# Performance work log

Hardware: AMD Instinct MI355X
Metric: run time of the kernel (lower is better)

## Reference

```python
import jax, jax.numpy as jnp
import numpy as np

B = 1
L_IMG, L_TMP, L_TXT = 1024, 1024, 256
D, H, HD, MLP = 1024, 16, 64, 4096
L = L_TXT + L_IMG + L_TMP
EPS = 1e-6
ATTN_SCALE = float(1.0 / np.sqrt(HD))


def setup_inputs() -> dict:
    key = jax.random.key(0)
    ks = jax.random.split(key, 12)
    s = 0.02  # keep activations stable
    return {
        'img': jax.random.normal(ks[0], (B, L_IMG, D), jnp.float32),
        'temporal': jax.random.normal(ks[1], (B, L_TMP, D), jnp.float32),
        'txt': jax.random.normal(ks[2], (B, L_TXT, D), jnp.float32),
        'vec': jax.random.normal(ks[3], (B, D), jnp.float32),
        'pe': jax.random.normal(ks[4], (B, 1, L, HD // 2, 2, 2), jnp.float32),
        'mod_w': jax.random.normal(ks[5], (3, D, 6 * D), jnp.float32) * s,
        'mod_b': jnp.zeros((3, 6 * D), jnp.float32),
        'qkv_w': jax.random.normal(ks[6], (3, D, 3 * D), jnp.float32) * s,
        'q_scale': jnp.ones((3, HD), jnp.float32),
        'k_scale': jnp.ones((3, HD), jnp.float32),
        'proj_w': jax.random.normal(ks[7], (3, D, D), jnp.float32) * s,
        'proj_b': jnp.zeros((3, D), jnp.float32),
        'mlp_w1': jax.random.normal(ks[8], (3, D, MLP), jnp.float32) * s,
        'mlp_b1': jnp.zeros((3, MLP), jnp.float32),
        'mlp_w2': jax.random.normal(ks[9], (3, MLP, D), jnp.float32) * s,
        'mlp_b2': jnp.zeros((3, D), jnp.float32),
    }


def _ln(x):
    # LayerNorm, elementwise_affine=False, eps=1e-6
    m = jnp.mean(x, axis=-1, keepdims=True)
    v = jnp.mean((x - m) ** 2, axis=-1, keepdims=True)
    return (x - m) * jax.lax.rsqrt(v + EPS)


def _rms(x, scale):
    # flux QKNorm RMSNorm with learnable per-head-dim scale
    return x * jax.lax.rsqrt(jnp.mean(x * x, axis=-1, keepdims=True) + EPS) * scale


def _rope(x, pe):
    # x: (B,H,L,HD), pe: (B,1,L,HD//2,2,2)
    xr = x.reshape(*x.shape[:-1], -1, 1, 2)
    out = pe[..., 0] * xr[..., 0] + pe[..., 1] * xr[..., 1]  # (B,H,L,HD//2,2)
    return out.reshape(x.shape)


def _forward(img, temporal, txt, vec, pe, mod_w, mod_b, qkv_w, q_scale, k_scale,
             proj_w, proj_b, mlp_w1, mlp_b1, mlp_w2, mlp_b2):
    sv = jax.nn.silu(vec)  # (B,D)

    def mods(i):
        m = (sv @ mod_w[i] + mod_b[i])[:, None, :]  # (B,1,6D)
        return jnp.split(m, 6, axis=-1)  # shift1, scale1, gate1, shift2, scale2, gate2

    def qkv_stream(x, i, shift1, scale1):
        xm = (1.0 + scale1) * _ln(x) + shift1
        qkv = (xm @ qkv_w[i]).reshape(x.shape[0], x.shape[1], 3, H, HD)
        q, k, v = jnp.moveaxis(qkv, 2, 0)  # each (B,Ls,H,HD)
        q = jnp.swapaxes(q, 1, 2)
        k = jnp.swapaxes(k, 1, 2)
        v = jnp.swapaxes(v, 1, 2)  # (B,H,Ls,HD)
        return _rms(q, q_scale[i]), _rms(k, k_scale[i]), v

    i_sh1, i_sc1, i_g1, i_sh2, i_sc2, i_g2 = mods(0)
    t_sh1, t_sc1, t_g1, t_sh2, t_sc2, t_g2 = mods(1)
    x_sh1, x_sc1, x_g1, x_sh2, x_sc2, x_g2 = mods(2)

    img_q, img_k, img_v = qkv_stream(img, 0, i_sh1, i_sc1)
    tmp_q, tmp_k, tmp_v = qkv_stream(temporal, 1, t_sh1, t_sc1)
    txt_q, txt_k, txt_v = qkv_stream(txt, 2, x_sh1, x_sc1)

    q = jnp.concatenate((txt_q, img_q, tmp_q), axis=2)
    k = jnp.concatenate((txt_k, img_k, tmp_k), axis=2)
    # NOTE: faithful to source bug: v concat uses temporal_q, not temporal_v
    v = jnp.concatenate((txt_v, img_v, tmp_q), axis=2)

    q = _rope(q, pe)
    k = _rope(k, pe)
    scores = jnp.einsum('bhqd,bhkd->bhqk', q, k) * ATTN_SCALE
    attn = jnp.einsum('bhqk,bhkd->bhqd', jax.nn.softmax(scores, axis=-1), v)
    attn = jnp.swapaxes(attn, 1, 2).reshape(attn.shape[0], L, H * HD)  # (B,L,D)

    txt_a = attn[:, :L_TXT]
    img_a = attn[:, L_TXT:L_TXT + L_IMG]
    tmp_a = attn[:, L_TXT + L_IMG:]

    def mlp(x, i):
        return jax.nn.gelu(x @ mlp_w1[i] + mlp_b1[i], approximate=True) @ mlp_w2[i] + mlp_b2[i]

    img = img + i_g1 * (img_a @ proj_w[0] + proj_b[0])
    img = img + i_g2 * mlp((1.0 + i_sc2) * _ln(img) + i_sh2, 0)
    temporal = temporal + t_g1 * (tmp_a @ proj_w[1] + proj_b[1])
    # NOTE: faithful to source bug: temporal_norm2 is applied to (updated) img
    temporal = temporal + t_g2 * mlp((1.0 + t_sc2) * _ln(img) + t_sh2, 1)
    txt = txt + x_g1 * (txt_a @ proj_w[2] + proj_b[2])
    txt = txt + x_g2 * mlp((1.0 + x_sc2) * _ln(txt) + x_sh2, 2)
    return img, temporal, txt


def reference(img, temporal, txt, vec, pe, mod_w, mod_b, qkv_w, q_scale, k_scale,
              proj_w, proj_b, mlp_w1, mlp_b1, mlp_w2, mlp_b2):
    return _forward(img, temporal, txt, vec, pe, mod_w, mod_b, qkv_w, q_scale,
                    k_scale, proj_w, proj_b, mlp_w1, mlp_b1, mlp_w2, mlp_b2)
```

## Files before the change

### kernel.cpp

```cpp
#include <hip/hip_runtime.h>
#include <hip/hip_bf16.h>

#define L_TXT 256
#define L_IMG 1024
#define L_TMP 1024
#define LTOT  2304
#define DMODEL 1024
#define NH 16
#define HDIM 64
#define DMLP 4096
#define EPSV 1e-6f

typedef unsigned short ushort;
typedef __attribute__((ext_vector_type(8))) short short8b;
typedef __attribute__((ext_vector_type(8))) unsigned short ushort8v;
typedef __attribute__((ext_vector_type(4))) float f32x4;
typedef __attribute__((ext_vector_type(4))) unsigned short ushort4v;

#define MOD_OFF    ((size_t)0)
#define XM_OFF     ((size_t)73728)
#define QKV_OFF    ((size_t)4792320)
#define QB_OFF     ((size_t)18948096)
#define KB_OFF     ((size_t)23666688)
#define VTB_OFF    ((size_t)28385280)
#define ATT_OFF    ((size_t)33103872)
#define S1_OFF     ((size_t)37822464)
#define QKVWT_OFF  ((size_t)49356800)
#define PROJWT_OFF ((size_t)68231168)
#define W1T_OFF    ((size_t)74522624)
#define W2T_OFF    ((size_t)99688448)
#define W2T_END    ((size_t)124854272)

static __device__ __forceinline__ ushort f2bf(float x) {
    __hip_bfloat16 b = __float2bfloat16(x);
    return *reinterpret_cast<ushort*>(&b);
}
static __device__ __forceinline__ float bf2f(ushort u) {
    return __uint_as_float(((unsigned)u) << 16);
}

typedef __attribute__((address_space(1))) const unsigned char gas_t;
typedef __attribute__((address_space(3))) unsigned char las_t;
static __device__ __forceinline__ void gload16(const void* g, void* l) {
    __builtin_amdgcn_global_load_lds((gas_t*)g, (las_t*)l, 16, 0, 0);
}

__global__ __launch_bounds__(256) void k_wt_all(const float* __restrict__ vec,
                                                const float* __restrict__ modw,
                                                const float* __restrict__ modb,
                                                float* __restrict__ mod,
                                                const float* __restrict__ qkvw,
                                                const float* __restrict__ projw,
                                                const float* __restrict__ w1,
                                                const float* __restrict__ w2,
                                                ushort* __restrict__ qkvwt,
                                                ushort* __restrict__ projwt,
                                                ushort* __restrict__ w1t,
                                                ushort* __restrict__ w2t) {
    __shared__ float tb[32][33];
    __shared__ float svs[DMODEL];
    __shared__ float pl[8][128];
    int bid = blockIdx.x;
    int tid = threadIdx.x;
    if (bid < 144) {
        float4 vv = *reinterpret_cast<const float4*>(vec + tid*4);
        float4 sv4;
        sv4.x = vv.x / (1.0f + __expf(-vv.x));
        sv4.y = vv.y / (1.0f + __expf(-vv.y));
        sv4.z = vv.z / (1.0f + __expf(-vv.z));
        sv4.w = vv.w / (1.0f + __expf(-vv.w));
        *reinterpret_cast<float4*>(&svs[tid*4]) = sv4;
        __syncthreads();
        int g0 = bid * 128;
        int i  = g0 / 6144;
        int j0 = g0 - i * 6144;
        int jl = tid & 31, ko = tid >> 5;
        const float* wp = modw + (size_t)i * 1024 * 6144 + j0 + jl*4;
        float4 acc = {0.f,0.f,0.f,0.f};
        for (int kk = 0; kk < 128; kk++) {
            int k = kk*8 + ko;
            float4 wv = *reinterpret_cast<const float4*>(wp + (size_t)k * 6144);
            float s = svs[k];
            acc.x += s*wv.x; acc.y += s*wv.y; acc.z += s*wv.z; acc.w += s*wv.w;
        }
        pl[ko][jl*4+0] = acc.x; pl[ko][jl*4+1] = acc.y;
        pl[ko][jl*4+2] = acc.z; pl[ko][jl*4+3] = acc.w;
        __syncthreads();
        if (tid < 128) {
            float s = 0.f;
#pragma unroll
            for (int k = 0; k < 8; k++) s += pl[k][tid];
            mod[g0 + tid] = s + modb[g0 + tid];
        }
        return;
    }
    bid -= 144;
    const float* W; ushort* WT; int K, N;
    if (bid < 9216) {
        int s = bid / 3072, r = bid % 3072;
        K = 1024; N = 3072;
        W = qkvw + (size_t)s * K * N; WT = qkvwt + (size_t)s * N * K;
        bid = r;
    } else if (bid < 12288) {
        int b = bid - 9216; int s = b / 1024, r = b % 1024;
        K = 1024; N = 1024;
        W = projw + (size_t)s * K * N; WT = projwt + (size_t)s * N * K;
        bid = r;
    } else if (bid < 24576) {
        int b = bid - 12288; int s = b / 4096, r = b % 4096;
        K = 1024; N = 4096;
        W = w1 + (size_t)s * K * N; WT = w1t + (size_t)s * N * K;
        bid = r;
    } else {
        int b = bid - 24576; int s = b / 4096, r = b % 4096;
        K = 4096; N = 1024;
        W = w2 + (size_t)s * K * N; WT = w2t + (size_t)s * N * K;
        bid = r;
    }
    int nt = bid % (N >> 5), kt = bid / (N >> 5);
    int r = tid >> 5, c = tid & 31;
#pragma unroll
    for (int i = 0; i < 4; i++)
        tb[r + i*8][c] = W[(size_t)(kt*32 + r + i*8) * N + nt*32 + c];
    __syncthreads();
#pragma unroll
    for (int i = 0; i < 4; i++)
        WT[(size_t)(nt*32 + r + i*8) * K + kt*32 + c] = f2bf(tb[c][r + i*8]);
}

__global__ __launch_bounds__(256) void k_wt_slice(const float* __restrict__ W,
                                                  ushort* __restrict__ WT,
                                                  int K, int N) {
    int nt = blockIdx.x, kt = blockIdx.y;
    __shared__ float tb[32][33];
    int r = threadIdx.x >> 5, c = threadIdx.x & 31;
#pragma unroll
    for (int i = 0; i < 4; i++)
        tb[r + i*8][c] = W[(size_t)(kt*32 + r + i*8) * N + nt*32 + c];
    __syncthreads();
#pragma unroll
    for (int i = 0; i < 4; i++)
        WT[(size_t)(nt*32 + r + i*8) * K + kt*32 + c] = f2bf(tb[c][r + i*8]);
}

__global__ __launch_bounds__(256) void k_ln_mod1(const float* __restrict__ img,
                                                 const float* __restrict__ tmp,
                                                 const float* __restrict__ txt,
                                                 const float* __restrict__ mod,
                                                 ushort* __restrict__ xm) {
    int l = blockIdx.x;
    const float* src; int strm;
    if (l < L_TXT)              { src = txt + (size_t)l * DMODEL;            strm = 2; }
    else if (l < L_TXT + L_IMG) { src = img + (size_t)(l - L_TXT) * DMODEL;  strm = 0; }
    else                        { src = tmp + (size_t)(l - L_TXT - L_IMG) * DMODEL; strm = 1; }

    int d = threadIdx.x * 4;
    float4 x = *reinterpret_cast<const float4*>(src + d);
    float s  = x.x + x.y + x.z + x.w;
    float s2 = x.x*x.x + x.y*x.y + x.z*x.z + x.w*x.w;
#pragma unroll
    for (int o = 32; o > 0; o >>= 1) { s += __shfl_xor(s, o); s2 += __shfl_xor(s2, o); }
    __shared__ float red[8];
    int wave = threadIdx.x >> 6, lane = threadIdx.x & 63;
    if (lane == 0) { red[wave*2] = s; red[wave*2+1] = s2; }
    __syncthreads();
    if (threadIdx.x == 0) {
        float a = 0.f, b = 0.f;
        for (int w = 0; w < 4; w++) { a += red[w*2]; b += red[w*2+1]; }
        red[0] = a; red[1] = b;
    }
    __syncthreads();
    float mean = red[0] * (1.0f/DMODEL);
    float var  = red[1] * (1.0f/DMODEL) - mean*mean;
    float inv  = rsqrtf(var + EPSV);

    const float* sh = mod + strm*6144;
    const float* sc = sh + 1024;
    float4 shv = *reinterpret_cast<const float4*>(sh + d);
    float4 scv = *reinterpret_cast<const float4*>(sc + d);
    ushort4v o;
    o.x = f2bf((1.f+scv.x)*((x.x-mean)*inv) + shv.x);
    o.y = f2bf((1.f+scv.y)*((x.y-mean)*inv) + shv.y);
    o.z = f2bf((1.f+scv.z)*((x.z-mean)*inv) + shv.z);
    o.w = f2bf((1.f+scv.w)*((x.w-mean)*inv) + shv.w);
    *reinterpret_cast<ushort4v*>(xm + (size_t)l*DMODEL + d) = o;
}

__global__ __launch_bounds__(256) void k_ln_mod2(const float* __restrict__ src,
                                                 const float* __restrict__ sh,
                                                 const float* __restrict__ sc,
                                                 ushort* __restrict__ out) {
    int r = blockIdx.x;
    const float* srow = src + (size_t)r * DMODEL;
    int d = threadIdx.x * 4;
    float4 x = *reinterpret_cast<const float4*>(srow + d);
    float s  = x.x + x.y + x.z + x.w;
    float s2 = x.x*x.x + x.y*x.y + x.z*x.z + x.w*x.w;
#pragma unroll
    for (int o = 32; o > 0; o >>= 1) { s += __shfl_xor(s, o); s2 += __shfl_xor(s2, o); }
    __shared__ float red[8];
    int wave = threadIdx.x >> 6, lane = threadIdx.x & 63;
    if (lane == 0) { red[wave*2] = s; red[wave*2+1] = s2; }
    __syncthreads();
    if (threadIdx.x == 0) {
        float a = 0.f, b = 0.f;
        for (int w = 0; w < 4; w++) { a += red[w*2]; b += red[w*2+1]; }
        red[0] = a; red[1] = b;
    }
    __syncthreads();
    float mean = red[0] * (1.0f/DMODEL);
    float var  = red[1] * (1.0f/DMODEL) - mean*mean;
    float inv  = rsqrtf(var + EPSV);
    float4 shv = *reinterpret_cast<const float4*>(sh + d);
    float4 scv = *reinterpret_cast<const float4*>(sc + d);
    ushort4v o;
    o.x = f2bf((1.f+scv.x)*((x.x-mean)*inv) + shv.x);
    o.y = f2bf((1.f+scv.y)*((x.y-mean)*inv) + shv.y);
    o.z = f2bf((1.f+scv.z)*((x.z-mean)*inv) + shv.z);
    o.w = f2bf((1.f+scv.w)*((x.w-mean)*inv) + shv.w);
    *reinterpret_cast<ushort4v*>(out + (size_t)r*DMODEL + d) = o;
}

__device__ __forceinline__ float gelu_fast(float x) {
    return x / (1.0f + __expf(-1.5957691216057308f * (x + 0.044715f * x * x * x)));
}

template<int MODE, int BM, typename OutT>
__global__ __launch_bounds__(256) void k_gemm_ms(const ushort* __restrict__ A_t,
                                                 const ushort* __restrict__ A_i,
                                                 const ushort* __restrict__ A_m,
                                                 const ushort* __restrict__ BT,
                                                 const float* __restrict__ bias,
                                                 const float* __restrict__ res_t,
                                                 const float* __restrict__ res_i,
                                                 const float* __restrict__ res_m,
                                                 const float* __restrict__ mod, int gidx,
                                                 OutT* __restrict__ out_t,
                                                 OutT* __restrict__ out_i,
                                                 OutT* __restrict__ out_m,
                                                 int N, int K, int ry0) {
    constexpr int MI = BM / 32;
    const int brow = (ry0 + blockIdx.y) * BM;
    int s, lrow;
    if (brow < 256)       { s = 2; lrow = brow; }
    else if (brow < 1280) { s = 0; lrow = brow - 256; }
    else                  { s = 1; lrow = brow - 1280; }

    const ushort* A = (s==2 ? A_t : s==0 ? A_i : A_m) + (size_t)lrow * K;
    const ushort* BTs = BT + (size_t)s * N * K;
    const float* bi = bias ? bias + (size_t)s * N : nullptr;
    const float* resl = (MODE==2) ? ((s==2 ? res_t : s==0 ? res_i : res_m) + (size_t)lrow * N) : nullptr;
    const float* gate = (MODE==2) ? (mod + s*6144 + gidx*1024) : nullptr;
    OutT* Cl = (s==2 ? out_t : s==0 ? out_i : out_m) + (size_t)lrow * N;

    __shared__ ushort Asl[BM*64];
    __shared__ ushort Bsl[128*64];
    const int tid = threadIdx.x;
    const int lane = tid & 63, w = tid >> 6;
    const int wr = w >> 1, wc = w & 1;
    const int bn = blockIdx.x * 128;
    const int r15 = lane & 15, g4 = lane >> 4;

    f32x4 acc[MI][4];
#pragma unroll
    for (int i = 0; i < MI; i++)
#pragma unroll
        for (int j = 0; j < 4; j++) acc[i][j] = (f32x4){0.f,0.f,0.f,0.f};

    for (int k0 = 0; k0 < K; k0 += 64) {
#pragma unroll
        for (int i = 0; i < BM/32; i++) {
            int chunk = i*4 + w;
            int seg = chunk*64 + lane;
            int row = seg >> 3;
            int gs  = (seg & 7) ^ (row & 7);
            gload16(A + (size_t)row * K + k0 + gs*8, Asl + (size_t)chunk * 512);
        }
#pragma unroll
        for (int i = 0; i < 4; i++) {
            int chunk = i*4 + w;
            int seg = chunk*64 + lane;
            int row = seg >> 3;
            int gs  = (seg & 7) ^ (row & 7);
            gload16(BTs + (size_t)(bn + row) * K + k0 + gs*8, Bsl + (size_t)chunk * 512);
        }
        __syncthreads();
#pragma unroll
        for (int kk = 0; kk < 2; kk++) {
            short8b a[MI], b[4];
#pragma unroll
            for (int mi = 0; mi < MI; mi++) {
                int row = wr*(MI*16) + mi*16 + r15;
                int c   = kk*4 + g4;
                a[mi] = *reinterpret_cast<const short8b*>(&Asl[row*64 + ((c ^ (row & 7)))*8]);
            }
#pragma unroll
            for (int ni = 0; ni < 4; ni++) {
                int row = wc*64 + ni*16 + r15;
                int c   = kk*4 + g4;
                b[ni] = *reinterpret_cast<const short8b*>(&Bsl[row*64 + ((c ^ (row & 7)))*8]);
            }
#pragma unroll
            for (int mi = 0; mi < MI; mi++)
#pragma unroll
                for (int ni = 0; ni < 4; ni++)
                    acc[mi][ni] = __builtin_amdgcn_mfma_f32_16x16x32_bf16(a[mi], b[ni], acc[mi][ni], 0, 0, 0);
        }
        __syncthreads();
    }

#pragma unroll
    for (int mi = 0; mi < MI; mi++) {
#pragma unroll
        for (int ni = 0; ni < 4; ni++) {
            int col = bn + wc*64 + ni*16 + r15;
            float bv = bi ? bi[col] : 0.f;
#pragma unroll
            for (int r = 0; r < 4; r++) {
                int rr = wr*(MI*16) + mi*16 + g4*4 + r;
                float v = acc[mi][ni][r] + bv;
                if (MODE == 1) v = gelu_fast(v);
                if (MODE == 2) v = resl[(size_t)rr * N + col] + gate[col] * v;
                if (sizeof(OutT) == 2) Cl[(size_t)rr * N + col] = (OutT)f2bf(v);
                else                   Cl[(size_t)rr * N + col] = (OutT)v;
            }
        }
    }
}

__global__ __launch_bounds__(256) void k_qkvfin(const ushort* __restrict__ qkv,
                                                const float* __restrict__ pe,
                                                const float* __restrict__ qs,
                                                const float* __restrict__ ks,
                                                ushort* __restrict__ Q,
                                                ushort* __restrict__ K,
                                                ushort* __restrict__ Vt) {
    int wid  = (blockIdx.x * 256 + threadIdx.x) >> 6;
    int lane = threadIdx.x & 63;
    int l = wid >> 4;
    int h = wid & 15;
    int strm;
    if (l < L_TXT) strm = 2; else if (l < L_TXT + L_IMG) strm = 0; else strm = 1;

    const ushort* row = qkv + (size_t)l * 3 * DMODEL;
    float q = bf2f(row[h*HDIM + lane]);
    float k = bf2f(row[DMODEL + h*HDIM + lane]);
    float v = bf2f(row[2*DMODEL + h*HDIM + lane]);

    float sq = q*q, sk = k*k;
#pragma unroll
    for (int o = 32; o > 0; o >>= 1) { sq += __shfl_xor(sq, o); sk += __shfl_xor(sk, o); }
    float rq = q * rsqrtf(sq * (1.0f/HDIM) + EPSV) * qs[strm*HDIM + lane];
    float rk = k * rsqrtf(sk * (1.0f/HDIM) + EPSV) * ks[strm*HDIM + lane];

    float vout = (strm == 1) ? rq : v;

    float rq_p = __shfl_xor(rq, 1);
    float rk_p = __shfl_xor(rk, 1);
    float qe = (lane & 1) ? rq_p : rq;
    float qo = (lane & 1) ? rq : rq_p;
    float ke = (lane & 1) ? rk_p : rk;
    float ko = (lane & 1) ? rk : rk_p;
    const float* pel = pe + (size_t)l*128 + (lane >> 1)*4 + (lane & 1)*2;
    float qr = pel[0]*qe + pel[1]*qo;
    float kr = pel[0]*ke + pel[1]*ko;

    size_t idx = ((size_t)h * LTOT + l) * HDIM + lane;
    Q[idx] = f2bf(qr);
    K[idx] = f2bf(kr);
    Vt[idx] = f2bf(vout);
}

__global__ __launch_bounds__(256) void k_vt(const ushort* __restrict__ Vt,
                                            ushort* __restrict__ VT) {
    int h  = blockIdx.x >> 5;
    int lt = blockIdx.x & 31;
    if (lt >= 36) return;
    h = blockIdx.x / 36; lt = blockIdx.x % 36;
    int l0 = lt * 64;
    __shared__ ushort tbuf[64][72];
    int tid = threadIdx.x;
    {
        int l = tid >> 2, dc = (tid & 3) * 16;
        const ushort* src = Vt + ((size_t)NH*0 + (size_t)h * LTOT + l0 + l) * 64 + dc;
        ushort8v a = *reinterpret_cast<const ushort8v*>(src);
        ushort8v b = *reinterpret_cast<const ushort8v*>(src + 8);
#pragma unroll
        for (int i = 0; i < 8; i++) { tbuf[l][dc+i] = a[i]; tbuf[l][dc+8+i] = b[i]; }
    }
    __syncthreads();
    {
        int d = tid >> 2, lc = (tid & 3) * 16;
        ushort8v a, b;
#pragma unroll
        for (int i = 0; i < 8; i++) { a[i] = tbuf[lc+i][d]; b[i] = tbuf[lc+8+i][d]; }
        ushort* dst = VT + ((size_t)h * 64 + d) * LTOT + l0 + lc;
        *reinterpret_cast<ushort8v*>(dst) = a;
        *reinterpret_cast<ushort8v*>(dst + 8) = b;
    }
}

__global__ __launch_bounds__(256) void k_attn_mfma(const ushort* __restrict__ Qb,
                                                   const ushort* __restrict__ Kb,
                                                   const ushort* __restrict__ VTb,
                                                   ushort* __restrict__ att) {
    const int tid = threadIdx.x;
    const int w = tid >> 6, lane = tid & 63;
    const int h  = blockIdx.x / 36;
    const int qt = blockIdx.x % 36;
    const int qbase = qt*64 + w*16;
    const int g = lane >> 4;
    const int q = lane & 15;

    __shared__ ushort Ksl[64*64];
    __shared__ ushort Vsl[64*64];
    __shared__ ushort plds[4][1024];
    ushort* P = plds[w];

    const ushort* Kg = Kb  + (size_t)h * LTOT * 64;
    const ushort* Vg = VTb + (size_t)h * 64 * LTOT;

    const ushort* qp = Qb + ((size_t)h * LTOT + qbase + q) * 64 + g*8;
    const short8b qf0 = *reinterpret_cast<const short8b*>(qp);
    const short8b qf1 = *reinterpret_cast<const short8b*>(qp + 32);

    f32x4 out[4];
#pragma unroll
    for (int d = 0; d < 4; d++) out[d] = (f32x4){0.f,0.f,0.f,0.f};
    float m = -1e30f, lsum = 0.f;

    for (int kv0 = 0; kv0 < LTOT; kv0 += 64) {
#pragma unroll
        for (int i = 0; i < 2; i++) {
            int seg = i*256 + tid;
            int row = seg >> 3;
            int gs  = (seg & 7) ^ (row & 7);
            gload16(Kg + (size_t)(kv0 + row)*64 + gs*8, Ksl + (size_t)(i*256 + w*64)*8);
            gload16(Vg + (size_t)row*LTOT + kv0 + gs*8, Vsl + (size_t)(i*256 + w*64)*8);
        }
        __syncthreads();

        f32x4 s[4];
#pragma unroll
        for (int ks = 0; ks < 4; ks++) {
            int r = ks*16 + q;
            short8b kf0 = *reinterpret_cast<const short8b*>(&Ksl[r*64 + ((g     ^ (r & 7)))*8]);
            short8b kf1 = *reinterpret_cast<const short8b*>(&Ksl[r*64 + (((4+g) ^ (r & 7)))*8]);
            f32x4 acc = (f32x4){0.f,0.f,0.f,0.f};
            acc = __builtin_amdgcn_mfma_f32_16x16x32_bf16(kf0, qf0, acc, 0, 0, 0);
            acc = __builtin_amdgcn_mfma_f32_16x16x32_bf16(kf1, qf1, acc, 0, 0, 0);
            s[ks] = acc;
        }
        float tmax = -1e30f;
#pragma unroll
        for (int ks = 0; ks < 4; ks++)
#pragma unroll
            for (int r = 0; r < 4; r++) tmax = fmaxf(tmax, s[ks][r]);
        tmax = fmaxf(tmax, __shfl_xor(tmax, 16));
        tmax = fmaxf(tmax, __shfl_xor(tmax, 32));
        float newm = fmaxf(m, tmax * 0.125f);
        float c = __expf(m - newm);
        float p[16];
        float tsum = 0.f;
#pragma unroll
        for (int ks = 0; ks < 4; ks++)
#pragma unroll
            for (int r = 0; r < 4; r++) {
                float pv = __expf(s[ks][r] * 0.125f - newm);
                p[ks*4+r] = pv;
                tsum += pv;
            }
        tsum += __shfl_xor(tsum, 16);
        tsum += __shfl_xor(tsum, 32);
        lsum = lsum * c + tsum;
        m = newm;
#pragma unroll
        for (int d = 0; d < 4; d++) out[d] *= c;

#pragma unroll
        for (int ks = 0; ks < 4; ks++) {
            ushort4v pk;
            pk.x = f2bf(p[ks*4+0]); pk.y = f2bf(p[ks*4+1]);
            pk.z = f2bf(p[ks*4+2]); pk.w = f2bf(p[ks*4+3]);
            int widx = (q*64 + ks*16 + g*4) ^ ((q & 7) << 3);
            *reinterpret_cast<ushort4v*>(&P[widx]) = pk;
        }
#pragma unroll
        for (int c2 = 0; c2 < 2; c2++) {
            int ridx = (q*64 + c2*32 + g*8) ^ ((q & 7) << 3);
            short8b pf = *reinterpret_cast<const short8b*>(&P[ridx]);
#pragma unroll
            for (int ds = 0; ds < 4; ds++) {
                int d = ds*16 + q;
                short8b vf = *reinterpret_cast<const short8b*>(&Vsl[d*64 + (((c2*4+g) ^ (d & 7)))*8]);
                out[ds] = __builtin_amdgcn_mfma_f32_16x16x32_bf16(vf, pf, out[ds], 0, 0, 0);
            }
        }
        __syncthreads();
    }

    float inv = 1.0f / lsum;
    ushort* orow = att + (size_t)(qbase + q) * DMODEL + h * HDIM;
#pragma unroll
    for (int ds = 0; ds < 4; ds++) {
        ushort4v o4;
        o4.x = f2bf(out[ds][0]*inv); o4.y = f2bf(out[ds][1]*inv);
        o4.z = f2bf(out[ds][2]*inv); o4.w = f2bf(out[ds][3]*inv);
        *reinterpret_cast<ushort4v*>(orow + ds*16 + g*4) = o4;
    }
}

extern "C" void kernel_launch(void* const* d_in, const int* in_sizes, int n_in,
                              void* d_out, int out_size, void* d_ws, size_t ws_size,
                              hipStream_t stream) {
    const float* img  = (const float*)d_in[0];
    const float* tmp  = (const float*)d_in[1];
    const float* txt  = (const float*)d_in[2];
    const float* vec  = (const float*)d_in[3];
    const float* pe   = (const float*)d_in[4];
    const float* modw = (const float*)d_in[5];
    const float* modb = (const float*)d_in[6];
    const float* qkvw = (const float*)d_in[7];
    const float* qsc  = (const float*)d_in[8];
    const float* ksc  = (const float*)d_in[9];
    const float* projw= (const float*)d_in[10];
    const float* projb= (const float*)d_in[11];
    const float* w1   = (const float*)d_in[12];
    const float* b1   = (const float*)d_in[13];
    const float* w2   = (const float*)d_in[14];
    const float* b2   = (const float*)d_in[15];

    char* wsb = (char*)d_ws;
    float*  mod    = (float*) (wsb + MOD_OFF);
    ushort* xm     = (ushort*)(wsb + XM_OFF);
    ushort* qkv    = (ushort*)(wsb + QKV_OFF);
    ushort* t1     = (ushort*)(wsb + QKV_OFF);
    ushort* Qb     = (ushort*)(wsb + QB_OFF);
    ushort* Kb     = (ushort*)(wsb + KB_OFF);
    ushort* VTb    = (ushort*)(wsb + VTB_OFF);
    ushort* vtmp   = (ushort*)(wsb + ATT_OFF);
    ushort* att    = (ushort*)(wsb + ATT_OFF);
    float*  s1     = (float*) (wsb + S1_OFF);
    ushort* qkvwt  = (ushort*)(wsb + QKVWT_OFF);
    ushort* projwt = (ushort*)(wsb + PROJWT_OFF);
    ushort* w1t    = (ushort*)(wsb + W1T_OFF);

    const bool bigws = ws_size >= W2T_END;
    ushort* w2t = bigws ? (ushort*)(wsb + W2T_OFF) : w1t;

    float* out_img = (float*)d_out;
    float* out_tmp = out_img + (size_t)L_IMG * DMODEL;
    float* out_txt = out_tmp + (size_t)L_TMP * DMODEL;

    int wt_blocks = bigws ? (144 + 24576 + 12288) : (144 + 24576);
    k_wt_all<<<wt_blocks, 256, 0, stream>>>(vec, modw, modb, mod,
                                            qkvw, projw, w1, w2,
                                            qkvwt, projwt, w1t, w2t);
    k_ln_mod1<<<LTOT, 256, 0, stream>>>(img, tmp, txt, mod, xm);

    k_gemm_ms<0, 128, ushort><<<dim3(24, 18), 256, 0, stream>>>(
        xm, xm + (size_t)256*DMODEL, xm + (size_t)1280*DMODEL,
        qkvwt, nullptr, nullptr, nullptr, nullptr, nullptr, 0,
        qkv, qkv + (size_t)256*3072, qkv + (size_t)1280*3072, 3072, DMODEL, 0);

    k_qkvfin<<<9216, 256, 0, stream>>>(qkv, pe, qsc, ksc, Qb, Kb, vtmp);
    k_vt<<<NH*36, 256, 0, stream>>>(vtmp, VTb);
    k_attn_mfma<<<NH*36, 256, 0, stream>>>(Qb, Kb, VTb, att);

    k_gemm_ms<2, 64, float><<<dim3(8, 36), 256, 0, stream>>>(
        att, att + (size_t)256*DMODEL, att + (size_t)1280*DMODEL,
        projwt, projb, txt, img, tmp, mod, 2,
        s1, s1 + (size_t)256*DMODEL, s1 + (size_t)1280*DMODEL, DMODEL, DMODEL, 0);

    k_ln_mod2<<<L_TXT, 256, 0, stream>>>(s1,                        mod + 2*6144 + 3*1024, mod + 2*6144 + 4*1024, xm);
    k_ln_mod2<<<L_IMG, 256, 0, stream>>>(s1 + (size_t)256*DMODEL,   mod + 0*6144 + 3*1024, mod + 0*6144 + 4*1024, xm + (size_t)256*DMODEL);
    k_gemm_ms<1, 128, ushort><<<dim3(32, 10), 256, 0, stream>>>(
        xm, xm + (size_t)256*DMODEL, xm + (size_t)1280*DMODEL,
        w1t, b1, nullptr, nullptr, nullptr, nullptr, 0,
        t1, t1 + (size_t)256*DMLP, t1, DMLP, DMODEL, 0);
    if (!bigws) {
        k_wt_slice<<<dim3(32, 128), 256, 0, stream>>>(w2,                          w1t,                          DMLP, DMODEL);
        k_wt_slice<<<dim3(32, 128), 256, 0, stream>>>(w2 + (size_t)2*DMLP*DMODEL,  w1t + (size_t)2*DMLP*DMODEL,  DMLP, DMODEL);
    }
    k_gemm_ms<2, 64, float><<<dim3(8, 20), 256, 0, stream>>>(
        t1, t1 + (size_t)256*DMLP, t1,
        w2t, b2, s1, s1 + (size_t)256*DMODEL, s1 + (size_t)1280*DMODEL, mod, 5,
        out_txt, out_img, out_tmp, DMODEL, DMLP, 0);

    k_ln_mod2<<<L_TMP, 256, 0, stream>>>(out_img, mod + 1*6144 + 3*1024, mod + 1*6144 + 4*1024, xm + (size_t)1280*DMODEL);
    k_gemm_ms<1, 128, ushort><<<dim3(32, 8), 256, 0, stream>>>(
        xm, xm + (size_t)256*DMODEL, xm + (size_t)1280*DMODEL,
        w1t, b1, nullptr, nullptr, nullptr, nullptr, 0,
        t1, t1, t1, DMLP, DMODEL, 10);
    if (!bigws) {
        k_wt_slice<<<dim3(32, 128), 256, 0, stream>>>(w2 + (size_t)DMLP*DMODEL, w1t + (size_t)DMLP*DMODEL, DMLP, DMODEL);
    }
    k_gemm_ms<2, 64, float><<<dim3(8, 16), 256, 0, stream>>>(
        t1, t1, t1,
        w2t, b2, s1, s1, s1 + (size_t)1280*DMODEL, mod, 5,
        out_txt, out_img, out_tmp, DMODEL, DMLP, 20);
}
```

Measured before the change: 356.7 us.

## Widen weight transpose tiles, fuse V transpose, merge LN launches, double-buffer attention

The weight conversion kernels now use 64x64 tiles with float4 loads and 16-byte bf16 stores instead of 32x32 scalar tiles. The V transpose is folded into the QKV finalize kernel through an LDS buffer, which removes the separate k_vt launch and the intermediate round trip. The two LN-modulation launches are merged into one. The attention kernel double-buffers its K/V LDS tiles, prefetching the next tile while computing the current one, and adds s_setprio hints around the MFMA sections. Together these target transpose bandwidth, launch count and load latency in attention, at the cost of more LDS per block and fewer threads in qkvfin.

Measured after the change: 354.8 us. About the same (-0.5%).

```diff
diff --git a/kernel.cpp b/kernel.cpp
--- a/kernel.cpp
+++ b/kernel.cpp
@@ -45,24 +45,24 @@
     __builtin_amdgcn_global_load_lds((gas_t*)g, (las_t*)l, 16, 0, 0);
 }
 
-__global__ __launch_bounds__(256) void k_wt_all(const float* __restrict__ vec,
-                                                const float* __restrict__ modw,
-                                                const float* __restrict__ modb,
-                                                float* __restrict__ mod,
-                                                const float* __restrict__ qkvw,
-                                                const float* __restrict__ projw,
-                                                const float* __restrict__ w1,
-                                                const float* __restrict__ w2,
-                                                ushort* __restrict__ qkvwt,
-                                                ushort* __restrict__ projwt,
-                                                ushort* __restrict__ w1t,
-                                                ushort* __restrict__ w2t) {
-    __shared__ float tb[32][33];
-    __shared__ float svs[DMODEL];
-    __shared__ float pl[8][128];
+__global__ __launch_bounds__(256) void k_conv(const float* __restrict__ vec,
+                                              const float* __restrict__ modw,
+                                              const float* __restrict__ modb,
+                                              float* __restrict__ mod,
+                                              const float* __restrict__ qkvw,
+                                              const float* __restrict__ projw,
+                                              const float* __restrict__ w1,
+                                              const float* __restrict__ w2,
+                                              ushort* __restrict__ qkvwt,
+                                              ushort* __restrict__ projwt,
+                                              ushort* __restrict__ w1t,
+                                              ushort* __restrict__ w2t) {
+    __shared__ float tb[64][65];
     int bid = blockIdx.x;
     int tid = threadIdx.x;
     if (bid < 144) {
+        __shared__ float svs[DMODEL];
+        __shared__ float pl[8][128];
         float4 vv = *reinterpret_cast<const float4*>(vec + tid*4);
         float4 sv4;
         sv4.x = vv.x / (1.0f + __expf(-vv.x));
@@ -94,53 +94,74 @@
         }
         return;
     }
-    bid -= 144;
-    const float* W; ushort* WT; int K, N;
-    if (bid < 9216) {
-        int s = bid / 3072, r = bid % 3072;
-        K = 1024; N = 3072;
+    int b = bid - 144;
+    const float* W; ushort* WT; int K, N, nt, kt;
+    if (b < 2304) {
+        int s = b / 768, r = b % 768;
+        K = 1024; N = 3072; nt = r % 48; kt = r / 48;
         W = qkvw + (size_t)s * K * N; WT = qkvwt + (size_t)s * N * K;
-        bid = r;
-    } else if (bid < 12288) {
-        int b = bid - 9216; int s = b / 1024, r = b % 1024;
-        K = 1024; N = 1024;
+    } else if (b < 3072) {
+        b -= 2304; int s = b / 256, r = b % 256;
+        K = 1024; N = 1024; nt = r % 16; kt = r / 16;
         W = projw + (size_t)s * K * N; WT = projwt + (size_t)s * N * K;
-        bid = r;
-    } else if (bid < 24576) {
-        int b = bid - 12288; int s = b / 4096, r = b % 4096;
-        K = 1024; N = 4096;
+    } else if (b < 6144) {
+        b -= 3072; int s = b / 1024, r = b % 1024;
+        K = 1024; N = 4096; nt = r % 64; kt = r / 64;
         W = w1 + (size_t)s * K * N; WT = w1t + (size_t)s * N * K;
-        bid = r;
     } else {
-        int b = bid - 24576; int s = b / 4096, r = b % 4096;
-        K = 4096; N = 1024;
+        b -= 6144; int s = b / 1024, r = b % 1024;
+        K = 4096; N = 1024; nt = r % 16; kt = r / 16;
         W = w2 + (size_t)s * K * N; WT = w2t + (size_t)s * N * K;
-        bid = r;
-    }
-    int nt = bid % (N >> 5), kt = bid / (N >> 5);
-    int r = tid >> 5, c = tid & 31;
-#pragma unroll
-    for (int i = 0; i < 4; i++)
-        tb[r + i*8][c] = W[(size_t)(kt*32 + r + i*8) * N + nt*32 + c];
-    __syncthreads();
-#pragma unroll
-    for (int i = 0; i < 4; i++)
-        WT[(size_t)(nt*32 + r + i*8) * K + kt*32 + c] = f2bf(tb[c][r + i*8]);
-}
-
-__global__ __launch_bounds__(256) void k_wt_slice(const float* __restrict__ W,
-                                                  ushort* __restrict__ WT,
-                                                  int K, int N) {
-    int nt = blockIdx.x, kt = blockIdx.y;
-    __shared__ float tb[32][33];
-    int r = threadIdx.x >> 5, c = threadIdx.x & 31;
-#pragma unroll
-    for (int i = 0; i < 4; i++)
-        tb[r + i*8][c] = W[(size_t)(kt*32 + r + i*8) * N + nt*32 + c];
-    __syncthreads();
-#pragma unroll
-    for (int i = 0; i < 4; i++)
-        WT[(size_t)(nt*32 + r + i*8) * K + kt*32 + c] = f2bf(tb[c][r + i*8]);
+    }
+    {
+        int r = tid >> 4, c4 = (tid & 15) * 4;
+#pragma unroll
+        for (int i = 0; i < 4; i++) {
+            float4 v = *reinterpret_cast<const float4*>(W + (size_t)(kt*64 + r + i*16) * N + nt*64 + c4);
+            tb[r + i*16][c4+0] = v.x; tb[r + i*16][c4+1] = v.y;
+            tb[r + i*16][c4+2] = v.z; tb[r + i*16][c4+3] = v.w;
+        }
+    }
+    __syncthreads();
+    {
+        int n = tid >> 2, ks = (tid & 3) * 16;
+        ushort8v u0, u1;
+#pragma unroll
+        for (int i = 0; i < 8; i++) u0[i] = f2bf(tb[ks+i][n]);
+#pragma unroll
+        for (int i = 0; i < 8; i++) u1[i] = f2bf(tb[ks+8+i][n]);
+        ushort* dst = WT + (size_t)(nt*64 + n) * K + kt*64 + ks;
+        *reinterpret_cast<ushort8v*>(dst)     = u0;
+        *reinterpret_cast<ushort8v*>(dst + 8) = u1;
+    }
+}
+
+__global__ __launch_bounds__(256) void k_conv_slice(const float* __restrict__ W,
+                                                    ushort* __restrict__ WT,
+                                                    int K, int N) {
+    __shared__ float tb[64][65];
+    int nt = blockIdx.x, kt = blockIdx.y, tid = threadIdx.x;
+    {
+        int r = tid >> 4, c4 = (tid & 15) * 4;
+#pragma unroll
+        for (int i = 0; i < 4; i++) {
+            float4 v = *reinterpret_cast<const float4*>(W + (size_t)(kt*64 + r + i*16) * N + nt*64 + c4);
+            tb[r + i*16][c4+0] = v.x; tb[r + i*16][c4+1] = v.y;
+            tb[r + i*16][c4+2] = v.z; tb[r + i*16][c4+3] = v.w;
+        }
+    }
+    __syncthreads();
+    {
+        int n = tid >> 2, ks = (tid & 3) * 16;
+        ushort8v u0, u1;
+#pragma unroll
+        for (int i = 0; i < 8; i++) u0[i] = f2bf(tb[ks+i][n]);
+#pragma unroll
+        for (int i = 0; i < 8; i++) u1[i] = f2bf(tb[ks+8+i][n]);
+        ushort* dst = WT + (size_t)(nt*64 + n) * K + kt*64 + ks;
+        *reinterpret_cast<ushort8v*>(dst)     = u0;
+        *reinterpret_cast<ushort8v*>(dst + 8) = u1;
+    }
 }
 
 __global__ __launch_bounds__(256) void k_ln_mod1(const float* __restrict__ img,
@@ -219,6 +240,43 @@
     o.z = f2bf((1.f+scv.z)*((x.z-mean)*inv) + shv.z);
     o.w = f2bf((1.f+scv.w)*((x.w-mean)*inv) + shv.w);
     *reinterpret_cast<ushort4v*>(out + (size_t)r*DMODEL + d) = o;
+}
+
+__global__ __launch_bounds__(256) void k_ln_modg(const float* __restrict__ s1,
+                                                 const float* __restrict__ mod,
+                                                 ushort* __restrict__ xm) {
+    int row = blockIdx.x;
+    int strm = row < 256 ? 2 : 0;
+    const float* srow = s1 + (size_t)row * DMODEL;
+    int d = threadIdx.x * 4;
+    float4 x = *reinterpret_cast<const float4*>(srow + d);
+    float s  = x.x + x.y + x.z + x.w;
+    float s2 = x.x*x.x + x.y*x.y + x.z*x.z + x.w*x.w;
+#pragma unroll
+    for (int o = 32; o > 0; o >>= 1) { s += __shfl_xor(s, o); s2 += __shfl_xor(s2, o); }
+    __shared__ float red[8];
+    int wave = threadIdx.x >> 6, lane = threadIdx.x & 63;
+    if (lane == 0) { red[wave*2] = s; red[wave*2+1] = s2; }
+    __syncthreads();
+    if (threadIdx.x == 0) {
+        float a = 0.f, b = 0.f;
+        for (int w = 0; w < 4; w++) { a += red[w*2]; b += red[w*2+1]; }
+        red[0] = a; red[1] = b;
+    }
+    __syncthreads();
+    float mean = red[0] * (1.0f/DMODEL);
+    float var  = red[1] * (1.0f/DMODEL) - mean*mean;
+    float inv  = rsqrtf(var + EPSV);
+    const float* sh = mod + strm*6144 + 3*1024;
+    const float* sc = mod + strm*6144 + 4*1024;
+    float4 shv = *reinterpret_cast<const float4*>(sh + d);
+    float4 scv = *reinterpret_cast<const float4*>(sc + d);
+    ushort4v o;
+    o.x = f2bf((1.f+scv.x)*((x.x-mean)*inv) + shv.x);
+    o.y = f2bf((1.f+scv.y)*((x.y-mean)*inv) + shv.y);
+    o.z = f2bf((1.f+scv.z)*((x.z-mean)*inv) + shv.z);
+    o.w = f2bf((1.f+scv.w)*((x.w-mean)*inv) + shv.w);
+    *reinterpret_cast<ushort4v*>(xm + (size_t)row*DMODEL + d) = o;
 }
 
 __device__ __forceinline__ float gelu_fast(float x) {
@@ -334,69 +392,57 @@
                                                 const float* __restrict__ ks,
                                                 ushort* __restrict__ Q,
                                                 ushort* __restrict__ K,
-                                                ushort* __restrict__ Vt) {
-    int wid  = (blockIdx.x * 256 + threadIdx.x) >> 6;
-    int lane = threadIdx.x & 63;
-    int l = wid >> 4;
-    int h = wid & 15;
-    int strm;
-    if (l < L_TXT) strm = 2; else if (l < L_TXT + L_IMG) strm = 0; else strm = 1;
-
-    const ushort* row = qkv + (size_t)l * 3 * DMODEL;
-    float q = bf2f(row[h*HDIM + lane]);
-    float k = bf2f(row[DMODEL + h*HDIM + lane]);
-    float v = bf2f(row[2*DMODEL + h*HDIM + lane]);
-
-    float sq = q*q, sk = k*k;
-#pragma unroll
-    for (int o = 32; o > 0; o >>= 1) { sq += __shfl_xor(sq, o); sk += __shfl_xor(sk, o); }
-    float rq = q * rsqrtf(sq * (1.0f/HDIM) + EPSV) * qs[strm*HDIM + lane];
-    float rk = k * rsqrtf(sk * (1.0f/HDIM) + EPSV) * ks[strm*HDIM + lane];
-
-    float vout = (strm == 1) ? rq : v;
-
-    float rq_p = __shfl_xor(rq, 1);
-    float rk_p = __shfl_xor(rk, 1);
-    float qe = (lane & 1) ? rq_p : rq;
-    float qo = (lane & 1) ? rq : rq_p;
-    float ke = (lane & 1) ? rk_p : rk;
-    float ko = (lane & 1) ? rk : rk_p;
-    const float* pel = pe + (size_t)l*128 + (lane >> 1)*4 + (lane & 1)*2;
-    float qr = pel[0]*qe + pel[1]*qo;
-    float kr = pel[0]*ke + pel[1]*ko;
-
-    size_t idx = ((size_t)h * LTOT + l) * HDIM + lane;
-    Q[idx] = f2bf(qr);
-    K[idx] = f2bf(kr);
-    Vt[idx] = f2bf(vout);
-}
-
-__global__ __launch_bounds__(256) void k_vt(const ushort* __restrict__ Vt,
-                                            ushort* __restrict__ VT) {
-    int h  = blockIdx.x >> 5;
-    int lt = blockIdx.x & 31;
-    if (lt >= 36) return;
-    h = blockIdx.x / 36; lt = blockIdx.x % 36;
-    int l0 = lt * 64;
-    __shared__ ushort tbuf[64][72];
-    int tid = threadIdx.x;
+                                                ushort* __restrict__ VT) {
+    const int tid = threadIdx.x;
+    const int w = tid >> 6, lane = tid & 63;
+    const int h  = blockIdx.x / 36;
+    const int l0 = (blockIdx.x % 36) * 64;
+    __shared__ ushort vbuf[64][65];
+
+    for (int it = 0; it < 16; it++) {
+        int ll = it*4 + w;
+        int l = l0 + ll;
+        int strm;
+        if (l < L_TXT) strm = 2; else if (l < L_TXT + L_IMG) strm = 0; else strm = 1;
+        const ushort* row = qkv + (size_t)l * 3 * DMODEL + h*HDIM + lane;
+        float q = bf2f(row[0]);
+        float k = bf2f(row[DMODEL]);
+        float v = bf2f(row[2*DMODEL]);
+
+        float sq = q*q, sk = k*k;
+#pragma unroll
+        for (int o = 32; o > 0; o >>= 1) { sq += __shfl_xor(sq, o); sk += __shfl_xor(sk, o); }
+        float rq = q * rsqrtf(sq * (1.0f/HDIM) + EPSV) * qs[strm*HDIM + lane];
+        float rk = k * rsqrtf(sk * (1.0f/HDIM) + EPSV) * ks[strm*HDIM + lane];
+
+        float vout = (strm == 1) ? rq : v;
+
+        float rq_p = __shfl_xor(rq, 1);
+        float rk_p = __shfl_xor(rk, 1);
+        float qe = (lane & 1) ? rq_p : rq;
+        float qo = (lane & 1) ? rq : rq_p;
+        float ke = (lane & 1) ? rk_p : rk;
+        float ko = (lane & 1) ? rk : rk_p;
+        const float* pel = pe + (size_t)l*128 + (lane >> 1)*4 + (lane & 1)*2;
+        float qr = pel[0]*qe + pel[1]*qo;
+        float kr = pel[0]*ke + pel[1]*ko;
+
+        size_t idx = ((size_t)h * LTOT + l) * HDIM + lane;
+        Q[idx] = f2bf(qr);
+        K[idx] = f2bf(kr);
+        vbuf[ll][lane] = f2bf(vout);
+    }
+    __syncthreads();
     {
-        int l = tid >> 2, dc = (tid & 3) * 16;
-        const ushort* src = Vt + ((size_t)NH*0 + (size_t)h * LTOT + l0 + l) * 64 + dc;
-        ushort8v a = *reinterpret_cast<const ushort8v*>(src);
-        ushort8v b = *reinterpret_cast<const ushort8v*>(src + 8);
-#pragma unroll
-        for (int i = 0; i < 8; i++) { tbuf[l][dc+i] = a[i]; tbuf[l][dc+8+i] = b[i]; }
-    }
-    __syncthreads();
-    {
-        int d = tid >> 2, lc = (tid & 3) * 16;
-        ushort8v a, b;
-#pragma unroll
-        for (int i = 0; i < 8; i++) { a[i] = tbuf[lc+i][d]; b[i] = tbuf[lc+8+i][d]; }
-        ushort* dst = VT + ((size_t)h * 64 + d) * LTOT + l0 + lc;
-        *reinterpret_cast<ushort8v*>(dst) = a;
-        *reinterpret_cast<ushort8v*>(dst + 8) = b;
+        int d = tid >> 2, ls = (tid & 3) * 16;
+        ushort8v u0, u1;
+#pragma unroll
+        for (int i = 0; i < 8; i++) u0[i] = vbuf[ls+i][d];
+#pragma unroll
+        for (int i = 0; i < 8; i++) u1[i] = vbuf[ls+8+i][d];
+        ushort* dst = VT + ((size_t)h * 64 + d) * LTOT + l0 + ls;
+        *reinterpret_cast<ushort8v*>(dst)     = u0;
+        *reinterpret_cast<ushort8v*>(dst + 8) = u1;
     }
 }
 
@@ -412,8 +458,8 @@
     const int g = lane >> 4;
     const int q = lane & 15;
 
-    __shared__ ushort Ksl[64*64];
-    __shared__ ushort Vsl[64*64];
+    __shared__ ushort Ksl[2][64*64];
+    __shared__ ushort Vsl[2][64*64];
     __shared__ ushort plds[4][1024];
     ushort* P = plds[w];
 
@@ -429,28 +475,43 @@
     for (int d = 0; d < 4; d++) out[d] = (f32x4){0.f,0.f,0.f,0.f};
     float m = -1e30f, lsum = 0.f;
 
-    for (int kv0 = 0; kv0 < LTOT; kv0 += 64) {
-#pragma unroll
-        for (int i = 0; i < 2; i++) {
-            int seg = i*256 + tid;
-            int row = seg >> 3;
-            int gs  = (seg & 7) ^ (row & 7);
-            gload16(Kg + (size_t)(kv0 + row)*64 + gs*8, Ksl + (size_t)(i*256 + w*64)*8);
-            gload16(Vg + (size_t)row*LTOT + kv0 + gs*8, Vsl + (size_t)(i*256 + w*64)*8);
-        }
+#pragma unroll
+    for (int i = 0; i < 2; i++) {
+        int seg = i*256 + tid;
+        int row = seg >> 3;
+        int gs  = (seg & 7) ^ (row & 7);
+        gload16(Kg + (size_t)row*64 + gs*8, &Ksl[0][(size_t)(i*256 + w*64)*8]);
+        gload16(Vg + (size_t)row*LTOT + gs*8, &Vsl[0][(size_t)(i*256 + w*64)*8]);
+    }
+
+    for (int t = 0; t < 36; t++) {
+        const int cb = t & 1;
         __syncthreads();
+        if (t < 35) {
+            int kvn = (t+1) * 64;
+#pragma unroll
+            for (int i = 0; i < 2; i++) {
+                int seg = i*256 + tid;
+                int row = seg >> 3;
+                int gs  = (seg & 7) ^ (row & 7);
+                gload16(Kg + (size_t)(kvn + row)*64 + gs*8, &Ksl[cb^1][(size_t)(i*256 + w*64)*8]);
+                gload16(Vg + (size_t)row*LTOT + kvn + gs*8, &Vsl[cb^1][(size_t)(i*256 + w*64)*8]);
+            }
+        }
 
         f32x4 s[4];
+        __builtin_amdgcn_s_setprio(1);
 #pragma unroll
         for (int ks = 0; ks < 4; ks++) {
             int r = ks*16 + q;
-            short8b kf0 = *reinterpret_cast<const short8b*>(&Ksl[r*64 + ((g     ^ (r & 7)))*8]);
-            short8b kf1 = *reinterpret_cast<const short8b*>(&Ksl[r*64 + (((4+g) ^ (r & 7)))*8]);
+            short8b kf0 = *reinterpret_cast<const short8b*>(&Ksl[cb][r*64 + ((g     ^ (r & 7)))*8]);
+            short8b kf1 = *reinterpret_cast<const short8b*>(&Ksl[cb][r*64 + (((4+g) ^ (r & 7)))*8]);
             f32x4 acc = (f32x4){0.f,0.f,0.f,0.f};
             acc = __builtin_amdgcn_mfma_f32_16x16x32_bf16(kf0, qf0, acc, 0, 0, 0);
             acc = __builtin_amdgcn_mfma_f32_16x16x32_bf16(kf1, qf1, acc, 0, 0, 0);
             s[ks] = acc;
         }
+        __builtin_amdgcn_s_setprio(0);
         float tmax = -1e30f;
 #pragma unroll
         for (int ks = 0; ks < 4; ks++)
@@ -485,6 +546,7 @@
             int widx = (q*64 + ks*16 + g*4) ^ ((q & 7) << 3);
             *reinterpret_cast<ushort4v*>(&P[widx]) = pk;
         }
+        __builtin_amdgcn_s_setprio(1);
 #pragma unroll
         for (int c2 = 0; c2 < 2; c2++) {
             int ridx = (q*64 + c2*32 + g*8) ^ ((q & 7) << 3);
@@ -492,11 +554,11 @@
 #pragma unroll
             for (int ds = 0; ds < 4; ds++) {
                 int d = ds*16 + q;
-                short8b vf = *reinterpret_cast<const short8b*>(&Vsl[d*64 + (((c2*4+g) ^ (d & 7)))*8]);
+                short8b vf = *reinterpret_cast<const short8b*>(&Vsl[cb][d*64 + (((c2*4+g) ^ (d & 7)))*8]);
                 out[ds] = __builtin_amdgcn_mfma_f32_16x16x32_bf16(vf, pf, out[ds], 0, 0, 0);
             }
         }
-        __syncthreads();
+        __builtin_amdgcn_s_setprio(0);
     }
 
     float inv = 1.0f / lsum;
@@ -538,7 +600,6 @@
     ushort* Qb     = (ushort*)(wsb + QB_OFF);
     ushort* Kb     = (ushort*)(wsb + KB_OFF);
     ushort* VTb    = (ushort*)(wsb + VTB_OFF);
-    ushort* vtmp   = (ushort*)(wsb + ATT_OFF);
     ushort* att    = (ushort*)(wsb + ATT_OFF);
     float*  s1     = (float*) (wsb + S1_OFF);
     ushort* qkvwt  = (ushort*)(wsb + QKVWT_OFF);
@@ -552,8 +613,8 @@
     float* out_tmp = out_img + (size_t)L_IMG * DMODEL;
     float* out_txt = out_tmp + (size_t)L_TMP * DMODEL;
 
-    int wt_blocks = bigws ? (144 + 24576 + 12288) : (144 + 24576);
-    k_wt_all<<<wt_blocks, 256, 0, stream>>>(vec, modw, modb, mod,
+    int conv_blocks = bigws ? (144 + 9216) : (144 + 6144);
+    k_conv<<<conv_blocks, 256, 0, stream>>>(vec, modw, modb, mod,
                                             qkvw, projw, w1, w2,
                                             qkvwt, projwt, w1t, w2t);
     k_ln_mod1<<<LTOT, 256, 0, stream>>>(img, tmp, txt, mod, xm);
@@ -563,8 +624,7 @@
         qkvwt, nullptr, nullptr, nullptr, nullptr, nullptr, 0,
         qkv, qkv + (size_t)256*3072, qkv + (size_t)1280*3072, 3072, DMODEL, 0);
 
-    k_qkvfin<<<9216, 256, 0, stream>>>(qkv, pe, qsc, ksc, Qb, Kb, vtmp);
-    k_vt<<<NH*36, 256, 0, stream>>>(vtmp, VTb);
+    k_qkvfin<<<NH*36, 256, 0, stream>>>(qkv, pe, qsc, ksc, Qb, Kb, VTb);
     k_attn_mfma<<<NH*36, 256, 0, stream>>>(Qb, Kb, VTb, att);
 
     k_gemm_ms<2, 64, float><<<dim3(8, 36), 256, 0, stream>>>(
@@ -572,15 +632,14 @@
         projwt, projb, txt, img, tmp, mod, 2,
         s1, s1 + (size_t)256*DMODEL, s1 + (size_t)1280*DMODEL, DMODEL, DMODEL, 0);
 
-    k_ln_mod2<<<L_TXT, 256, 0, stream>>>(s1,                        mod + 2*6144 + 3*1024, mod + 2*6144 + 4*1024, xm);
-    k_ln_mod2<<<L_IMG, 256, 0, stream>>>(s1 + (size_t)256*DMODEL,   mod + 0*6144 + 3*1024, mod + 0*6144 + 4*1024, xm + (size_t)256*DMODEL);
+    k_ln_modg<<<1280, 256, 0, stream>>>(s1, mod, xm);
     k_gemm_ms<1, 128, ushort><<<dim3(32, 10), 256, 0, stream>>>(
         xm, xm + (size_t)256*DMODEL, xm + (size_t)1280*DMODEL,
         w1t, b1, nullptr, nullptr, nullptr, nullptr, 0,
         t1, t1 + (size_t)256*DMLP, t1, DMLP, DMODEL, 0);
     if (!bigws) {
-        k_wt_slice<<<dim3(32, 128), 256, 0, stream>>>(w2,                          w1t,                          DMLP, DMODEL);
-        k_wt_slice<<<dim3(32, 128), 256, 0, stream>>>(w2 + (size_t)2*DMLP*DMODEL,  w1t + (size_t)2*DMLP*DMODEL,  DMLP, DMODEL);
+        k_conv_slice<<<dim3(16, 64), 256, 0, stream>>>(w2,                          w1t,                          DMLP, DMODEL);
+        k_conv_slice<<<dim3(16, 64), 256, 0, stream>>>(w2 + (size_t)2*DMLP*DMODEL,  w1t + (size_t)2*DMLP*DMODEL,  DMLP, DMODEL);
     }
     k_gemm_ms<2, 64, float><<<dim3(8, 20), 256, 0, stream>>>(
         t1, t1 + (size_t)256*DMLP, t1,
@@ -593,7 +652,7 @@
         w1t, b1, nullptr, nullptr, nullptr, nullptr, 0,
         t1, t1, t1, DMLP, DMODEL, 10);
     if (!bigws) {
-        k_wt_slice<<<dim3(32, 128), 256, 0, stream>>>(w2 + (size_t)DMLP*DMODEL, w1t + (size_t)DMLP*DMODEL, DMLP, DMODEL);
+        k_conv_slice<<<dim3(16, 64), 256, 0, stream>>>(w2 + (size_t)DMLP*DMODEL, w1t + (size_t)DMLP*DMODEL, DMLP, DMODEL);
     }
     k_gemm_ms<2, 64, float><<<dim3(8, 16), 256, 0, stream>>>(
         t1, t1, t1,
```
